# Kernel optimization log

Hardware: AMD Instinct MI355X
Metric: run time of the kernel (lower is better)

The kernel has to match this reference:

```python
import jax, jax.numpy as jnp
import numpy as np

N_NODES = 10000
N_EDGES = 320000
HIDDEN = 16      # hidden_state_size
MSG = 64         # message_size
EDGE_FEAT = 32


def setup_inputs() -> dict:
    key = jax.random.key(0)
    ks = jax.random.split(key, 8)
    node_features = jax.random.normal(ks[0], (N_NODES, HIDDEN), dtype=jnp.float32)
    edge_features = jax.random.normal(ks[1], (N_EDGES, EDGE_FEAT), dtype=jnp.float32)
    edge_sources = jax.random.randint(ks[2], (N_EDGES,), 0, N_NODES, dtype=jnp.int32)
    edge_targets = jax.random.randint(ks[3], (N_EDGES,), 0, N_NODES, dtype=jnp.int32)
    hidden = jax.random.normal(ks[4], (N_NODES, HIDDEN), dtype=jnp.float32)
    initial = jax.random.normal(ks[5], (N_NODES, HIDDEN), dtype=jnp.float32)
    # Dense(edge_feat -> MSG*HIDDEN), glorot-ish scale
    W = jax.random.normal(ks[6], (EDGE_FEAT, MSG * HIDDEN), dtype=jnp.float32) / np.float32(np.sqrt(EDGE_FEAT))
    b = jnp.zeros((MSG * HIDDEN,), dtype=jnp.float32)
    return {
        "node_features": node_features,
        "edge_features": edge_features,
        "edge_sources": edge_sources,
        "edge_targets": edge_targets,
        "hidden": hidden,
        "initial": initial,
        "W": W,
        "b": b,
    }


def reference(node_features, edge_features, edge_sources, edge_targets, hidden, initial, W, b):
    # Per edge: edge_mat = Dense(edge_feat) reshaped (MSG, HIDDEN);
    # message = edge_mat @ hidden[source]; aggregate = sum over incoming edges per target node.
    num_nodes = node_features.shape[0]
    edge_mat = (edge_features @ W + b).reshape(-1, MSG, HIDDEN)  # [E, M, H]
    neigh = hidden[edge_sources]                                  # [E, H] gather
    messages = jnp.einsum("emh,eh->em", edge_mat, neigh)         # [E, M] batched matvec
    out = jax.ops.segment_sum(messages, edge_targets, num_segments=num_nodes)  # [N, M]
    return out
```

## Files before the change

kernel.cpp:

```cpp
#include <hip/hip_runtime.h>
#include <hip/hip_bf16.h>

#define N_NODES 10000
#define N_EDGES 320000
#define HIDDEN 16
#define MSG 64
#define EDGE_FEAT 32
#define KSTEPS 17
#define KTOT 544

typedef __attribute__((ext_vector_type(8))) short bf16x8;
typedef __attribute__((ext_vector_type(4))) float f32x4;

static __device__ __forceinline__ ushort f2bfu(float x) {
    __hip_bfloat16 h = __float2bfloat16(x);
    return *reinterpret_cast<ushort*>(&h);
}

__global__ void zero_prep(const float* __restrict__ W, const float* __restrict__ bias,
                          ushort* __restrict__ WrB, int* __restrict__ cnt,
                          float4* __restrict__ out4, int n4) {
    if (blockIdx.x < KSTEPS) {
        const int ks   = blockIdx.x;
        const int nt   = threadIdx.x >> 6;
        const int lane = threadIdx.x & 63;
        const int g    = lane >> 4;
        const int n    = nt * 16 + (lane & 15);
        ushort* dst = WrB + (((size_t)ks * 4 + nt) * 64 + lane) * 8;
        #pragma unroll
        for (int i = 0; i < 8; ++i) {
            const int k = ks * 32 + g * 8 + i;
            float v;
            if (k < 512)      v = W[(size_t)(k >> 4) * 1024 + n * 16 + (k & 15)];
            else if (k < 528) v = bias[n * 16 + (k - 512)];
            else              v = 0.0f;
            dst[i] = f2bfu(v);
        }
    } else if (blockIdx.x < KSTEPS + 40) {
        const int idx = (blockIdx.x - KSTEPS) * 256 + threadIdx.x;
        if (idx < N_NODES) cnt[idx] = 0;
    } else {
        const int i = (blockIdx.x - KSTEPS - 40) * 256 + threadIdx.x;
        if (i < n4) out4[i] = make_float4(0.f, 0.f, 0.f, 0.f);
    }
}

__global__ __launch_bounds__(256) void rank_kernel(const int* __restrict__ tgt,
                                                   int* __restrict__ cnt,
                                                   int* __restrict__ rank) {
    const int e = blockIdx.x * 256 + threadIdx.x;
    if (e < N_EDGES) rank[e] = atomicAdd(&cnt[tgt[e]], 1);
}

__global__ __launch_bounds__(1024) void scan_kernel(const int* __restrict__ cnt,
                                                    int* __restrict__ starts) {
    __shared__ int wsum[16];
    __shared__ int wbase[16];
    const int tid  = threadIdx.x;
    const int lane = tid & 63;
    const int wv   = tid >> 6;
    int c[10];
    int s = 0;
    #pragma unroll
    for (int j = 0; j < 10; ++j) {
        const int idx = tid * 10 + j;
        c[j] = (idx < N_NODES) ? cnt[idx] : 0;
        s += c[j];
    }
    int v = s;
    #pragma unroll
    for (int d = 1; d < 64; d <<= 1) {
        const int u = __shfl_up(v, d);
        if (lane >= d) v += u;
    }
    if (lane == 63) wsum[wv] = v;
    __syncthreads();
    if (tid < 16) {
        const int w = wsum[tid];
        int iv = w;
        #pragma unroll
        for (int d = 1; d < 16; d <<= 1) {
            const int u = __shfl_up(iv, d);
            if (tid >= d) iv += u;
        }
        wbase[tid] = iv - w;
    }
    __syncthreads();
    int running = wbase[wv] + (v - s);
    #pragma unroll
    for (int j = 0; j < 10; ++j) {
        const int idx = tid * 10 + j;
        if (idx < N_NODES) starts[idx] = running;
        running += c[j];
    }
    if (tid == 1023) starts[N_NODES] = N_EDGES;
}

__global__ __launch_bounds__(256) void build_iperm(
    const int* __restrict__ tgt, const int* __restrict__ rank,
    const int* __restrict__ starts, int* __restrict__ iperm) {
    const int e = blockIdx.x * 256 + threadIdx.x;
    if (e < N_EDGES) iperm[starts[tgt[e]] + rank[e]] = e;
}

__global__ __launch_bounds__(256) void fused_msg(
    const int*    __restrict__ iperm,
    const int*    __restrict__ tgt,
    const int*    __restrict__ src,
    const float*  __restrict__ ef,
    const float*  __restrict__ hidden,
    const ushort* __restrict__ WrB,
    float*        __restrict__ out)
{
    __shared__ float ef_s[64][36];
    __shared__ float neigh_s[64][20];
    __shared__ int   tgt_s[64];
    __shared__ float msg_s[64][68];

    const int tid = threadIdx.x;
    const int s0  = blockIdx.x * 64;

    const int e = iperm[s0 + (tid >> 2)];
    {
        const int h4 = (tid & 3) * 4;
        const int sn = src[e];
        *(float4*)&neigh_s[tid >> 2][h4] = *(const float4*)(hidden + (size_t)sn * HIDDEN + h4);
    }
    {
        const int f8 = (tid & 3) * 8;
        const float* p = ef + (size_t)e * EDGE_FEAT + f8;
        *(float4*)&ef_s[tid >> 2][f8]     = *(const float4*)(p);
        *(float4*)&ef_s[tid >> 2][f8 + 4] = *(const float4*)(p + 4);
    }
    if (tid < 64) {
        ef_s[tid][32] = 1.0f;
        ef_s[tid][33] = 0.0f;
        tgt_s[tid] = tgt[iperm[s0 + tid]];
    }
    __syncthreads();

    const int wave  = tid >> 6;
    const int lane  = tid & 63;
    const int er    = lane & 15;
    const int g     = lane >> 4;
    const int e_loc = wave * 16 + er;
    const int h0    = (g & 1) * 8;
    const int fg    = g >> 1;

    float nb[8];
    #pragma unroll
    for (int j = 0; j < 8; ++j) nb[j] = neigh_s[e_loc][h0 + j];

    f32x4 acc0 = {0.f,0.f,0.f,0.f}, acc1 = acc0, acc2 = acc0, acc3 = acc0;
    const bf16x8* Bp = (const bf16x8*)WrB;
    #pragma unroll
    for (int ks = 0; ks < KSTEPS; ++ks) {
        const float a = ef_s[e_loc][2 * ks + fg];
        bf16x8 af;
        #pragma unroll
        for (int j = 0; j < 8; ++j) af[j] = (short)f2bfu(a * nb[j]);
        const bf16x8 b0 = Bp[(ks * 4 + 0) * 64 + lane];
        const bf16x8 b1 = Bp[(ks * 4 + 1) * 64 + lane];
        const bf16x8 b2 = Bp[(ks * 4 + 2) * 64 + lane];
        const bf16x8 b3 = Bp[(ks * 4 + 3) * 64 + lane];
        acc0 = __builtin_amdgcn_mfma_f32_16x16x32_bf16(af, b0, acc0, 0, 0, 0);
        acc1 = __builtin_amdgcn_mfma_f32_16x16x32_bf16(af, b1, acc1, 0, 0, 0);
        acc2 = __builtin_amdgcn_mfma_f32_16x16x32_bf16(af, b2, acc2, 0, 0, 0);
        acc3 = __builtin_amdgcn_mfma_f32_16x16x32_bf16(af, b3, acc3, 0, 0, 0);
    }

    #pragma unroll
    for (int r = 0; r < 4; ++r) {
        const int row = wave * 16 + g * 4 + r;
        msg_s[row][ 0 + er] = acc0[r];
        msg_s[row][16 + er] = acc1[r];
        msg_s[row][32 + er] = acc2[r];
        msg_s[row][48 + er] = acc3[r];
    }
    __syncthreads();

    const int c = tid & 63;
    const int rbase = (tid >> 6) * 16;
    float run = msg_s[rbase][c];
    int   cur = tgt_s[rbase];
    #pragma unroll
    for (int r = 1; r < 16; ++r) {
        const int   tg = tgt_s[rbase + r];
        const float m  = msg_s[rbase + r][c];
        if (tg != cur) {
            atomicAdd(out + (size_t)cur * MSG + c, run);
            cur = tg;
            run = m;
        } else {
            run += m;
        }
    }
    atomicAdd(out + (size_t)cur * MSG + c, run);
}

__global__ __launch_bounds__(256) void zero_out(float* __restrict__ p, int n4) {
    const int i = blockIdx.x * 256 + threadIdx.x;
    if (i < n4) ((float4*)p)[i] = make_float4(0.f, 0.f, 0.f, 0.f);
}

__global__ __launch_bounds__(256, 4) void msg_mfma(
    const float* __restrict__ ef, const int* __restrict__ src,
    const int* __restrict__ tgt, const float* __restrict__ hidden,
    const ushort* __restrict__ WrB, float* __restrict__ out)
{
    __shared__ float ef_s[64][36];
    __shared__ float neigh_s[64][20];
    __shared__ int   tgt_s[64];
    const int tid = threadIdx.x;
    const int e0  = blockIdx.x * 64;
    {
        const int e = tid >> 2, h4 = (tid & 3) * 4;
        const int s = src[e0 + e];
        *(float4*)&neigh_s[e][h4] = *(const float4*)(hidden + (size_t)s * HIDDEN + h4);
    }
    {
        const int e = tid >> 2, f8 = (tid & 3) * 8;
        const float* p = ef + (size_t)(e0 + e) * EDGE_FEAT + f8;
        *(float4*)&ef_s[e][f8]     = *(const float4*)(p);
        *(float4*)&ef_s[e][f8 + 4] = *(const float4*)(p + 4);
    }
    if (tid < 64) { ef_s[tid][32] = 1.0f; ef_s[tid][33] = 0.0f; tgt_s[tid] = tgt[e0 + tid]; }
    __syncthreads();
    const int wave = tid >> 6, lane = tid & 63;
    const int er = lane & 15, g = lane >> 4;
    const int e_loc = wave * 16 + er;
    const int h0 = (g & 1) * 8, fg = g >> 1;
    float nb[8];
    #pragma unroll
    for (int j = 0; j < 8; ++j) nb[j] = neigh_s[e_loc][h0 + j];
    f32x4 acc0 = {0.f,0.f,0.f,0.f}, acc1 = acc0, acc2 = acc0, acc3 = acc0;
    const bf16x8* Bp = (const bf16x8*)WrB;
    #pragma unroll
    for (int ks = 0; ks < KSTEPS; ++ks) {
        const float a = ef_s[e_loc][2 * ks + fg];
        bf16x8 af;
        #pragma unroll
        for (int j = 0; j < 8; ++j) af[j] = (short)f2bfu(a * nb[j]);
        const bf16x8 b0 = Bp[(ks * 4 + 0) * 64 + lane];
        const bf16x8 b1 = Bp[(ks * 4 + 1) * 64 + lane];
        const bf16x8 b2 = Bp[(ks * 4 + 2) * 64 + lane];
        const bf16x8 b3 = Bp[(ks * 4 + 3) * 64 + lane];
        acc0 = __builtin_amdgcn_mfma_f32_16x16x32_bf16(af, b0, acc0, 0, 0, 0);
        acc1 = __builtin_amdgcn_mfma_f32_16x16x32_bf16(af, b1, acc1, 0, 0, 0);
        acc2 = __builtin_amdgcn_mfma_f32_16x16x32_bf16(af, b2, acc2, 0, 0, 0);
        acc3 = __builtin_amdgcn_mfma_f32_16x16x32_bf16(af, b3, acc3, 0, 0, 0);
    }
    #pragma unroll
    for (int r = 0; r < 4; ++r) {
        const int t = tgt_s[wave * 16 + g * 4 + r];
        float* op = out + (size_t)t * MSG;
        atomicAdd(op +      er, acc0[r]);
        atomicAdd(op + 16 + er, acc1[r]);
        atomicAdd(op + 32 + er, acc2[r]);
        atomicAdd(op + 48 + er, acc3[r]);
    }
}

extern "C" void kernel_launch(void* const* d_in, const int* in_sizes, int n_in,
                              void* d_out, int out_size, void* d_ws, size_t ws_size,
                              hipStream_t stream) {
    const float* ef     = (const float*)d_in[1];
    const int*   src    = (const int*)d_in[2];
    const int*   tgt    = (const int*)d_in[3];
    const float* hidden = (const float*)d_in[4];
    const float* W      = (const float*)d_in[6];
    const float* bias   = (const float*)d_in[7];
    float* out = (float*)d_out;
    char*  ws  = (char*)d_ws;

    const size_t o_wrb    = 0;
    const size_t o_starts = 69632;
    const size_t o_cnt    = 109648;
    const size_t o_rank   = 149648;
    const size_t o_iperm  = 1429648;
    const size_t need     = o_iperm + 1280000;

    ushort* WrB = (ushort*)(ws + o_wrb);
    const int n4 = out_size / 4;

    if (ws_size >= need) {
        int* starts = (int*)(ws + o_starts);
        int* cnt    = (int*)(ws + o_cnt);
        int* rank   = (int*)(ws + o_rank);
        int* iperm  = (int*)(ws + o_iperm);

        const int zb_cnt = 40;
        const int zb_out = (n4 + 255) / 256;
        zero_prep<<<KSTEPS + zb_cnt + zb_out, 256, 0, stream>>>(W, bias, WrB, cnt,
                                                                (float4*)out, n4);
        rank_kernel<<<(N_EDGES + 255) / 256, 256, 0, stream>>>(tgt, cnt, rank);
        scan_kernel<<<1, 1024, 0, stream>>>(cnt, starts);
        build_iperm<<<(N_EDGES + 255) / 256, 256, 0, stream>>>(tgt, rank, starts, iperm);
        fused_msg<<<N_EDGES / 64, 256, 0, stream>>>(iperm, tgt, src, ef, hidden, WrB, out);
    } else {
        zero_prep<<<KSTEPS, 256, 0, stream>>>(W, bias, WrB, nullptr, nullptr, 0);
        zero_out<<<(n4 + 255) / 256, 256, 0, stream>>>(out, n4);
        msg_mfma<<<N_EDGES / 64, 256, 0, stream>>>(ef, src, tgt, hidden, WrB, out);
    }
}
```

Before: 89.98 us.

## Switch MFMA to fp16 with packed A-operand build and process 128 edges per block

```diff
diff --git a/kernel.cpp b/kernel.cpp
--- a/kernel.cpp
+++ b/kernel.cpp
@@ -7,15 +7,14 @@
 #define MSG 64
 #define EDGE_FEAT 32
 #define KSTEPS 17
-#define KTOT 544
-
-typedef __attribute__((ext_vector_type(8))) short bf16x8;
-typedef __attribute__((ext_vector_type(4))) float f32x4;
-
-static __device__ __forceinline__ ushort f2bfu(float x) {
-    __hip_bfloat16 h = __float2bfloat16(x);
-    return *reinterpret_cast<ushort*>(&h);
-}
+#define EPB 128
+
+typedef __attribute__((ext_vector_type(2))) _Float16 f16x2;
+typedef __attribute__((ext_vector_type(4))) _Float16 f16x4;
+typedef __attribute__((ext_vector_type(8))) _Float16 f16x8;
+typedef __attribute__((ext_vector_type(4))) float    f32x4;
+
+union H8 { f16x8 v; f16x2 p[4]; f16x4 q[2]; };
 
 __global__ void zero_prep(const float* __restrict__ W, const float* __restrict__ bias,
                           ushort* __restrict__ WrB, int* __restrict__ cnt,
@@ -34,7 +33,8 @@
             if (k < 512)      v = W[(size_t)(k >> 4) * 1024 + n * 16 + (k & 15)];
             else if (k < 528) v = bias[n * 16 + (k - 512)];
             else              v = 0.0f;
-            dst[i] = f2bfu(v);
+            const _Float16 hv = (_Float16)v;
+            dst[i] = *reinterpret_cast<const ushort*>(&hv);
         }
     } else if (blockIdx.x < KSTEPS + 40) {
         const int idx = (blockIdx.x - KSTEPS) * 256 + threadIdx.x;
@@ -112,79 +112,110 @@
     const ushort* __restrict__ WrB,
     float*        __restrict__ out)
 {
-    __shared__ float ef_s[64][36];
-    __shared__ float neigh_s[64][20];
-    __shared__ int   tgt_s[64];
-    __shared__ float msg_s[64][68];
+    __shared__ _Float16 ef_h[EPB][36];
+    __shared__ _Float16 nb_h[EPB][16];
+    __shared__ int      tgt_s[EPB];
+    __shared__ float    msg_s[EPB][68];
 
     const int tid = threadIdx.x;
-    const int s0  = blockIdx.x * 64;
-
-    const int e = iperm[s0 + (tid >> 2)];
+    const int s0  = blockIdx.x * EPB;
+
     {
-        const int h4 = (tid & 3) * 4;
-        const int sn = src[e];
-        *(float4*)&neigh_s[tid >> 2][h4] = *(const float4*)(hidden + (size_t)sn * HIDDEN + h4);
-    }
-    {
-        const int f8 = (tid & 3) * 8;
-        const float* p = ef + (size_t)e * EDGE_FEAT + f8;
-        *(float4*)&ef_s[tid >> 2][f8]     = *(const float4*)(p);
-        *(float4*)&ef_s[tid >> 2][f8 + 4] = *(const float4*)(p + 4);
-    }
-    if (tid < 64) {
-        ef_s[tid][32] = 1.0f;
-        ef_s[tid][33] = 0.0f;
-        tgt_s[tid] = tgt[iperm[s0 + tid]];
-    }
-    __syncthreads();
-
-    const int wave  = tid >> 6;
-    const int lane  = tid & 63;
-    const int er    = lane & 15;
-    const int g     = lane >> 4;
-    const int e_loc = wave * 16 + er;
-    const int h0    = (g & 1) * 8;
-    const int fg    = g >> 1;
-
-    float nb[8];
-    #pragma unroll
-    for (int j = 0; j < 8; ++j) nb[j] = neigh_s[e_loc][h0 + j];
-
-    f32x4 acc0 = {0.f,0.f,0.f,0.f}, acc1 = acc0, acc2 = acc0, acc3 = acc0;
-    const bf16x8* Bp = (const bf16x8*)WrB;
+        const int sl   = tid >> 1;
+        const int half = tid & 1;
+        const int e    = iperm[s0 + sl];
+        const int sn   = src[e];
+
+        const float4* ep = (const float4*)(ef + (size_t)e * EDGE_FEAT + half * 16);
+        const float4 v0 = ep[0], v1 = ep[1], v2 = ep[2], v3 = ep[3];
+        _Float16* dst = &ef_h[sl][half * 16];
+        *(f16x4*)(dst + 0)  = f16x4{(_Float16)v0.x, (_Float16)v0.y, (_Float16)v0.z, (_Float16)v0.w};
+        *(f16x4*)(dst + 4)  = f16x4{(_Float16)v1.x, (_Float16)v1.y, (_Float16)v1.z, (_Float16)v1.w};
+        *(f16x4*)(dst + 8)  = f16x4{(_Float16)v2.x, (_Float16)v2.y, (_Float16)v2.z, (_Float16)v2.w};
+        *(f16x4*)(dst + 12) = f16x4{(_Float16)v3.x, (_Float16)v3.y, (_Float16)v3.z, (_Float16)v3.w};
+
+        const float4* hp = (const float4*)(hidden + (size_t)sn * HIDDEN + half * 8);
+        const float4 h0 = hp[0], h1 = hp[1];
+        *(f16x8*)&nb_h[sl][half * 8] =
+            f16x8{(_Float16)h0.x, (_Float16)h0.y, (_Float16)h0.z, (_Float16)h0.w,
+                  (_Float16)h1.x, (_Float16)h1.y, (_Float16)h1.z, (_Float16)h1.w};
+
+        if (half) {
+            ef_h[sl][32] = (_Float16)1.0f;
+            ef_h[sl][33] = (_Float16)0.0f;
+            ef_h[sl][34] = (_Float16)0.0f;
+            ef_h[sl][35] = (_Float16)0.0f;
+        } else {
+            tgt_s[sl] = tgt[e];
+        }
+    }
+    __syncthreads();
+
+    const int wave = tid >> 6;
+    const int lane = tid & 63;
+    const int er   = lane & 15;
+    const int g    = lane >> 4;
+    const int eA   = wave * 32 + er;
+    const int eB   = eA + 16;
+    const int hoff = (g & 1) * 8;
+    const int fg   = g >> 1;
+
+    H8 nbA, nbB;
+    nbA.v = *(const f16x8*)&nb_h[eA][hoff];
+    nbB.v = *(const f16x8*)&nb_h[eB][hoff];
+
+    f32x4 aA0 = {0.f,0.f,0.f,0.f}, aA1 = aA0, aA2 = aA0, aA3 = aA0;
+    f32x4 aB0 = aA0, aB1 = aA0, aB2 = aA0, aB3 = aA0;
+    const f16x8* Bp = (const f16x8*)WrB;
+
     #pragma unroll
     for (int ks = 0; ks < KSTEPS; ++ks) {
-        const float a = ef_s[e_loc][2 * ks + fg];
-        bf16x8 af;
+        const f16x8 b0 = Bp[(ks * 4 + 0) * 64 + lane];
+        const f16x8 b1 = Bp[(ks * 4 + 1) * 64 + lane];
+        const f16x8 b2 = Bp[(ks * 4 + 2) * 64 + lane];
+        const f16x8 b3 = Bp[(ks * 4 + 3) * 64 + lane];
+
+        const _Float16 a_A = ef_h[eA][2 * ks + fg];
+        const _Float16 a_B = ef_h[eB][2 * ks + fg];
+        const f16x2 avA = {a_A, a_A};
+        const f16x2 avB = {a_B, a_B};
+        H8 afA, afB;
         #pragma unroll
-        for (int j = 0; j < 8; ++j) af[j] = (short)f2bfu(a * nb[j]);
-        const bf16x8 b0 = Bp[(ks * 4 + 0) * 64 + lane];
-        const bf16x8 b1 = Bp[(ks * 4 + 1) * 64 + lane];
-        const bf16x8 b2 = Bp[(ks * 4 + 2) * 64 + lane];
-        const bf16x8 b3 = Bp[(ks * 4 + 3) * 64 + lane];
-        acc0 = __builtin_amdgcn_mfma_f32_16x16x32_bf16(af, b0, acc0, 0, 0, 0);
-        acc1 = __builtin_amdgcn_mfma_f32_16x16x32_bf16(af, b1, acc1, 0, 0, 0);
-        acc2 = __builtin_amdgcn_mfma_f32_16x16x32_bf16(af, b2, acc2, 0, 0, 0);
-        acc3 = __builtin_amdgcn_mfma_f32_16x16x32_bf16(af, b3, acc3, 0, 0, 0);
+        for (int q = 0; q < 4; ++q) {
+            afA.p[q] = avA * nbA.p[q];
+            afB.p[q] = avB * nbB.p[q];
+        }
+        aA0 = __builtin_amdgcn_mfma_f32_16x16x32_f16(afA.v, b0, aA0, 0, 0, 0);
+        aA1 = __builtin_amdgcn_mfma_f32_16x16x32_f16(afA.v, b1, aA1, 0, 0, 0);
+        aA2 = __builtin_amdgcn_mfma_f32_16x16x32_f16(afA.v, b2, aA2, 0, 0, 0);
+        aA3 = __builtin_amdgcn_mfma_f32_16x16x32_f16(afA.v, b3, aA3, 0, 0, 0);
+        aB0 = __builtin_amdgcn_mfma_f32_16x16x32_f16(afB.v, b0, aB0, 0, 0, 0);
+        aB1 = __builtin_amdgcn_mfma_f32_16x16x32_f16(afB.v, b1, aB1, 0, 0, 0);
+        aB2 = __builtin_amdgcn_mfma_f32_16x16x32_f16(afB.v, b2, aB2, 0, 0, 0);
+        aB3 = __builtin_amdgcn_mfma_f32_16x16x32_f16(afB.v, b3, aB3, 0, 0, 0);
     }
 
     #pragma unroll
     for (int r = 0; r < 4; ++r) {
-        const int row = wave * 16 + g * 4 + r;
-        msg_s[row][ 0 + er] = acc0[r];
-        msg_s[row][16 + er] = acc1[r];
-        msg_s[row][32 + er] = acc2[r];
-        msg_s[row][48 + er] = acc3[r];
+        const int rowA = wave * 32 + g * 4 + r;
+        msg_s[rowA][ 0 + er] = aA0[r];
+        msg_s[rowA][16 + er] = aA1[r];
+        msg_s[rowA][32 + er] = aA2[r];
+        msg_s[rowA][48 + er] = aA3[r];
+        const int rowB = rowA + 16;
+        msg_s[rowB][ 0 + er] = aB0[r];
+        msg_s[rowB][16 + er] = aB1[r];
+        msg_s[rowB][32 + er] = aB2[r];
+        msg_s[rowB][48 + er] = aB3[r];
     }
     __syncthreads();
 
     const int c = tid & 63;
-    const int rbase = (tid >> 6) * 16;
+    const int rbase = (tid >> 6) * 32;
     float run = msg_s[rbase][c];
     int   cur = tgt_s[rbase];
     #pragma unroll
-    for (int r = 1; r < 16; ++r) {
+    for (int r = 1; r < 32; ++r) {
         const int   tg = tgt_s[rbase + r];
         const float m  = msg_s[rbase + r][c];
         if (tg != cur) {
@@ -234,21 +265,21 @@
     #pragma unroll
     for (int j = 0; j < 8; ++j) nb[j] = neigh_s[e_loc][h0 + j];
     f32x4 acc0 = {0.f,0.f,0.f,0.f}, acc1 = acc0, acc2 = acc0, acc3 = acc0;
-    const bf16x8* Bp = (const bf16x8*)WrB;
+    const f16x8* Bp = (const f16x8*)WrB;
     #pragma unroll
     for (int ks = 0; ks < KSTEPS; ++ks) {
         const float a = ef_s[e_loc][2 * ks + fg];
-        bf16x8 af;
+        f16x8 af;
         #pragma unroll
-        for (int j = 0; j < 8; ++j) af[j] = (short)f2bfu(a * nb[j]);
-        const bf16x8 b0 = Bp[(ks * 4 + 0) * 64 + lane];
-        const bf16x8 b1 = Bp[(ks * 4 + 1) * 64 + lane];
-        const bf16x8 b2 = Bp[(ks * 4 + 2) * 64 + lane];
-        const bf16x8 b3 = Bp[(ks * 4 + 3) * 64 + lane];
-        acc0 = __builtin_amdgcn_mfma_f32_16x16x32_bf16(af, b0, acc0, 0, 0, 0);
-        acc1 = __builtin_amdgcn_mfma_f32_16x16x32_bf16(af, b1, acc1, 0, 0, 0);
-        acc2 = __builtin_amdgcn_mfma_f32_16x16x32_bf16(af, b2, acc2, 0, 0, 0);
-        acc3 = __builtin_amdgcn_mfma_f32_16x16x32_bf16(af, b3, acc3, 0, 0, 0);
+        for (int j = 0; j < 8; ++j) af[j] = (_Float16)(a * nb[j]);
+        const f16x8 b0 = Bp[(ks * 4 + 0) * 64 + lane];
+        const f16x8 b1 = Bp[(ks * 4 + 1) * 64 + lane];
+        const f16x8 b2 = Bp[(ks * 4 + 2) * 64 + lane];
+        const f16x8 b3 = Bp[(ks * 4 + 3) * 64 + lane];
+        acc0 = __builtin_amdgcn_mfma_f32_16x16x32_f16(af, b0, acc0, 0, 0, 0);
+        acc1 = __builtin_amdgcn_mfma_f32_16x16x32_f16(af, b1, acc1, 0, 0, 0);
+        acc2 = __builtin_amdgcn_mfma_f32_16x16x32_f16(af, b2, acc2, 0, 0, 0);
+        acc3 = __builtin_amdgcn_mfma_f32_16x16x32_f16(af, b3, acc3, 0, 0, 0);
     }
     #pragma unroll
     for (int r = 0; r < 4; ++r) {
@@ -296,7 +327,7 @@
         rank_kernel<<<(N_EDGES + 255) / 256, 256, 0, stream>>>(tgt, cnt, rank);
         scan_kernel<<<1, 1024, 0, stream>>>(cnt, starts);
         build_iperm<<<(N_EDGES + 255) / 256, 256, 0, stream>>>(tgt, rank, starts, iperm);
-        fused_msg<<<N_EDGES / 64, 256, 0, stream>>>(iperm, tgt, src, ef, hidden, WrB, out);
+        fused_msg<<<N_EDGES / EPB, 256, 0, stream>>>(iperm, tgt, src, ef, hidden, WrB, out);
     } else {
         zero_prep<<<KSTEPS, 256, 0, stream>>>(W, bias, WrB, nullptr, nullptr, 0);
         zero_out<<<(n4 + 255) / 256, 256, 0, stream>>>(out, n4);
```

Result: faster. 85.83 us (-4.6%).
